# Performance work log

Measured on AMD Instinct MI355X. Metric: run time of the kernel, lower is better.

Reference implementation:

```python
import jax, jax.numpy as jnp
import numpy as np

B, TQ, TKV, D_MODEL, H, DQ, DV = 4, 2048, 2048, 1024, 16, 64, 64
DK = DQ

def setup_inputs() -> dict:
    key = jax.random.key(0)
    ks = jax.random.split(key, 8)
    s = 0.02
    return {
        "query_sequence": jax.random.normal(ks[0], (B, TQ, D_MODEL), jnp.float32),
        "key_value_sequence": jax.random.normal(ks[1], (B, TKV, D_MODEL), jnp.float32),
        "key_value_padding_mask": jnp.zeros((B, TKV), dtype=bool),
        "Wq": jax.random.normal(ks[2], (D_MODEL, H * DQ), jnp.float32) * s,
        "bq": jnp.zeros((H * DQ,), jnp.float32),
        "Wkv": jax.random.normal(ks[3], (D_MODEL, H * (DK + DV)), jnp.float32) * s,
        "bkv": jnp.zeros((H * (DK + DV),), jnp.float32),
        "Wo": jax.random.normal(ks[4], (H * DV, D_MODEL), jnp.float32) * s,
        "bo": jnp.zeros((D_MODEL,), jnp.float32),
        "apply_causal_mask": 1,
    }

def reference(query_sequence, key_value_sequence, key_value_padding_mask,
              Wq, bq, Wkv, bkv, Wo, bo, apply_causal_mask):
    b, tq, _ = query_sequence.shape
    tkv = key_value_sequence.shape[1]
    q = (query_sequence @ Wq + bq).reshape(b, tq, H, DQ)          # (B,Tq,H,Dq)
    kv = key_value_sequence @ Wkv + bkv
    k = kv[..., : H * DK].reshape(b, tkv, H, DK)                   # (B,Tkv,H,Dk)
    v = kv[..., H * DK :].reshape(b, tkv, H, DV)                   # (B,Tkv,H,Dv)
    scores = jnp.einsum("bqhd,bkhd->bhqk", q, k) / jnp.sqrt(jnp.float32(DK))
    neg_inf = jnp.float32(-jnp.inf)
    scores = jnp.where(key_value_padding_mask[:, None, None, :], neg_inf, scores)
    if apply_causal_mask:
        causal = jnp.tril(jnp.ones((tq, tkv), dtype=bool))
        scores = jnp.where(causal[None, None, :, :], scores, neg_inf)
    attn = jax.nn.softmax(scores, axis=-1)
    out = jnp.einsum("bhqk,bkhd->bqhd", attn, v).reshape(b, tq, H * DV)
    return out @ Wo + bo
```

## Files before the change

kernel.cpp:

```cpp
#include <hip/hip_runtime.h>
#include <hip/hip_bf16.h>

#define B_   4
#define TQ_  2048
#define TKV_ 2048
#define DM_  1024
#define H_   16
#define DH_  64

#define SC_FOLD 0.18033688011112042f

using f32x4  = __attribute__((ext_vector_type(4))) float;
using f32x16 = __attribute__((ext_vector_type(16))) float;
using s16x8  = __attribute__((ext_vector_type(8))) short;

static __device__ __forceinline__ unsigned short f2bf(float f) {
  union { float f; unsigned int u; } v; v.f = f;
  unsigned int r = v.u + 0x7FFFu + ((v.u >> 16) & 1u);
  return (unsigned short)(r >> 16);
}
static __device__ __forceinline__ unsigned int pk2(float a, float b) {
  unsigned int r;
  asm("v_cvt_pk_bf16_f32 %0, %1, %2" : "=v"(r) : "v"(a), "v"(b));
  return r;
}
static __device__ __forceinline__ float max3f(float a, float b, float c) {
  float r;
  asm("v_max3_f32 %0, %1, %2, %3" : "=v"(r) : "v"(a), "v"(b), "v"(c));
  return r;
}

#define GL16(g, l)                                                          \
  __builtin_amdgcn_global_load_lds(                                         \
      (const __attribute__((address_space(1))) unsigned int*)(g),           \
      (__attribute__((address_space(3))) unsigned int*)(l), 16, 0, 0)

static __device__ __forceinline__ void transpose_tile(
    const float* W, unsigned short* WT, int K, int N, int n0, int k0, float scale,
    float (*t)[65]) {
  int tx = threadIdx.x & 63, ty = threadIdx.x >> 6;
#pragma unroll
  for (int i = 0; i < 64; i += 4)
    t[ty + i][tx] = W[(size_t)(k0 + ty + i) * N + n0 + tx];
  __syncthreads();
#pragma unroll
  for (int i = 0; i < 64; i += 4)
    WT[(size_t)(n0 + ty + i) * K + k0 + tx] = f2bf(t[tx][ty + i] * scale);
}
static __device__ __forceinline__ void cast_gs(
    const float* in, unsigned short* out, int n4, int cb, int ncb) {
  for (int i = cb * 256 + threadIdx.x; i < n4; i += ncb * 256) {
    f32x4 v = *(const f32x4*)(in + (size_t)i * 4);
    unsigned long long u = (unsigned long long)pk2(v[0], v[1]) |
                           ((unsigned long long)pk2(v[2], v[3]) << 32);
    *(unsigned long long*)(out + (size_t)i * 4) = u;
  }
}

__global__ __launch_bounds__(256) void k_prep(
    const float* __restrict__ Wq, unsigned short* __restrict__ WqT,
    const float* __restrict__ Wkv, unsigned short* __restrict__ WkvT,
    const float* __restrict__ Wo, unsigned short* __restrict__ WoT,
    const float* __restrict__ xq, unsigned short* __restrict__ Aq,
    const float* __restrict__ xkv, unsigned short* __restrict__ Akv, int n4) {
  int bid = blockIdx.x;
  if (bid >= 3072) { cast_gs(xkv, Akv, n4, bid - 3072, 2048); return; }
  if (bid >= 1024) { cast_gs(xq, Aq, n4, bid - 1024, 2048); return; }
  __shared__ float t[64][65];
  if (bid < 256) {
    transpose_tile(Wq, WqT, 1024, 1024, (bid & 15) * 64, (bid >> 4) * 64, SC_FOLD, t);
  } else if (bid < 768) {
    int b2 = bid - 256;
    transpose_tile(Wkv, WkvT, 1024, 2048, (b2 & 31) * 64, (b2 >> 5) * 64, 1.0f, t);
  } else {
    int b2 = bid - 768;
    transpose_tile(Wo, WoT, 1024, 1024, (b2 & 15) * 64, (b2 >> 4) * 64, 1.0f, t);
  }
}

__global__ __launch_bounds__(256) void k_cast_bf16(
    const float* __restrict__ in, unsigned short* __restrict__ out, int n4) {
  cast_gs(in, out, n4, blockIdx.x, gridDim.x);
}

template <int MODE, int BN>
static __device__ __forceinline__ void gemm_body(
    const unsigned short* __restrict__ A, const unsigned short* __restrict__ BT,
    const float* __restrict__ bias, float bscale, unsigned short* __restrict__ out_a,
    unsigned short* __restrict__ out_b, float* __restrict__ out_f, int Kd,
    int bx, int by, unsigned short* As, unsigned short* Bs) {
  constexpr int NI = BN / 64;
  constexpr int NH = NI / 2;
  const int tid = threadIdx.x, lane = tid & 63, w = tid >> 6;
  const int wm = w >> 2, wn = w & 3;
  int m0 = by * 256, n0 = bx * BN;

  const int strow = tid >> 3;
  const int sx = ((tid & 7) << 4) ^ ((strow & 7) << 4);
  const char* gA = (const char*)(A + (size_t)(m0 + strow) * Kd) + sx;
  const char* gB = (const char*)(BT + (size_t)(n0 + strow) * Kd) + sx;
  char* lA = (char*)As;
  char* lB = (char*)Bs;

#define ST_A(bf, c, k0) \
  GL16(gA + ((size_t)(c) * 64 * Kd + (size_t)(k0)) * 2, lA + (bf) * 32768 + (c) * 8192 + tid * 16)
#define ST_B(bf, c, k0) \
  GL16(gB + ((size_t)(c) * 64 * Kd + (size_t)(k0)) * 2, lB + (bf) * (BN * 128) + (c) * 8192 + tid * 16)

  f32x4 acc[8][NI];
#pragma unroll
  for (int i = 0; i < 8; ++i)
#pragma unroll
    for (int j = 0; j < NI; ++j) acc[i][j] = (f32x4){0.f, 0.f, 0.f, 0.f};

  s16x8 afr[4][2], bfr[NI][2];
  const int arow = wm * 128 + (lane & 15);
  const int brow = wn * (NI * 16) + (lane & 15);
  const int fcol = (lane >> 4) * 16;

#define RD_A(bf, r) (*(const s16x8*)(lA + (bf) * 32768 + (r) * 128 + ((fcol + _kk * 64) ^ (((r) & 7) << 4))))
#define RD_B(bf, r) (*(const s16x8*)(lB + (bf) * (BN * 128) + (r) * 128 + ((fcol + _kk * 64) ^ (((r) & 7) << 4))))

  const int nT = Kd >> 6;

  ST_B(0, 0, 0); ST_B(0, 1, 0);
  if (BN == 256) { ST_B(0, 2, 0); ST_B(0, 3, 0); }
  ST_A(0, 0, 0); ST_A(0, 2, 0);
  ST_A(0, 1, 0); ST_A(0, 3, 0);
  asm volatile("s_waitcnt vmcnt(2)" ::: "memory");
  __builtin_amdgcn_s_barrier();

#pragma unroll 1
  for (int t = 0; t < nT; ++t) {
    const int cur = t & 1, nxt = cur ^ 1;
    const int k1 = (t + 1) << 6;
    const bool st = (t + 1 < nT);

#pragma unroll
    for (int mi = 0; mi < 4; ++mi)
#pragma unroll
      for (int _kk = 0; _kk < 2; ++_kk) afr[mi][_kk] = RD_A(cur, arow + mi * 16);
#pragma unroll
    for (int ni = 0; ni < NH; ++ni)
#pragma unroll
      for (int _kk = 0; _kk < 2; ++_kk) bfr[ni][_kk] = RD_B(cur, brow + ni * 16);
    if (st) { ST_B(nxt, 0, k1); ST_B(nxt, 1, k1); }
    __builtin_amdgcn_s_barrier();
    __builtin_amdgcn_s_setprio(1);
#pragma unroll
    for (int mi = 0; mi < 4; ++mi)
#pragma unroll
      for (int ni = 0; ni < NH; ++ni)
#pragma unroll
        for (int kk = 0; kk < 2; ++kk)
          acc[mi][ni] = __builtin_amdgcn_mfma_f32_16x16x32_bf16(afr[mi][kk], bfr[ni][kk], acc[mi][ni], 0, 0, 0);
    __builtin_amdgcn_s_setprio(0);
    __builtin_amdgcn_s_barrier();

#pragma unroll
    for (int ni = NH; ni < NI; ++ni)
#pragma unroll
      for (int _kk = 0; _kk < 2; ++_kk) bfr[ni][_kk] = RD_B(cur, brow + ni * 16);
    if (st) {
      if (BN == 256) { ST_B(nxt, 2, k1); ST_B(nxt, 3, k1); }
      else           { ST_A(nxt, 0, k1); ST_A(nxt, 2, k1); }
    }
    if (st) asm volatile("s_waitcnt vmcnt(4)" ::: "memory");
    else    asm volatile("s_waitcnt vmcnt(0)" ::: "memory");
    __builtin_amdgcn_s_barrier();
    __builtin_amdgcn_s_setprio(1);
#pragma unroll
    for (int mi = 0; mi < 4; ++mi)
#pragma unroll
      for (int ni = NH; ni < NI; ++ni)
#pragma unroll
        for (int kk = 0; kk < 2; ++kk)
          acc[mi][ni] = __builtin_amdgcn_mfma_f32_16x16x32_bf16(afr[mi][kk], bfr[ni][kk], acc[mi][ni], 0, 0, 0);
    __builtin_amdgcn_s_setprio(0);
    __builtin_amdgcn_s_barrier();

#pragma unroll
    for (int mi = 0; mi < 4; ++mi)
#pragma unroll
      for (int _kk = 0; _kk < 2; ++_kk) afr[mi][_kk] = RD_A(cur, arow + (mi + 4) * 16);
    if (st) {
      if (BN == 256) { ST_A(nxt, 0, k1); ST_A(nxt, 2, k1); }
      else           { ST_A(nxt, 1, k1); ST_A(nxt, 3, k1); }
    }
    __builtin_amdgcn_s_barrier();
    __builtin_amdgcn_s_setprio(1);
#pragma unroll
    for (int mi = 0; mi < 4; ++mi)
#pragma unroll
      for (int ni = 0; ni < NH; ++ni)
#pragma unroll
        for (int kk = 0; kk < 2; ++kk)
          acc[mi + 4][ni] = __builtin_amdgcn_mfma_f32_16x16x32_bf16(afr[mi][kk], bfr[ni][kk], acc[mi + 4][ni], 0, 0, 0);
    __builtin_amdgcn_s_setprio(0);
    __builtin_amdgcn_s_barrier();

    if (st && BN == 256) { ST_A(nxt, 1, k1); ST_A(nxt, 3, k1); }
    asm volatile("s_waitcnt vmcnt(2)" ::: "memory");
    __builtin_amdgcn_s_barrier();
    __builtin_amdgcn_s_setprio(1);
#pragma unroll
    for (int mi = 0; mi < 4; ++mi)
#pragma unroll
      for (int ni = NH; ni < NI; ++ni)
#pragma unroll
        for (int kk = 0; kk < 2; ++kk)
          acc[mi + 4][ni] = __builtin_amdgcn_mfma_f32_16x16x32_bf16(afr[mi][kk], bfr[ni][kk], acc[mi + 4][ni], 0, 0, 0);
    __builtin_amdgcn_s_setprio(0);
    __builtin_amdgcn_s_barrier();
  }

#pragma unroll
  for (int mi = 0; mi < 8; ++mi) {
#pragma unroll
    for (int ni = 0; ni < NI; ++ni) {
      int col = n0 + wn * (NI * 16) + ni * 16 + (lane & 15);
      int rbase = m0 + wm * 128 + mi * 16 + (lane >> 4) * 4;
      float bv = bias[col] * bscale;
      if (MODE == 1 && col >= H_ * DH_) {
        int c2 = col - H_ * DH_;
        int h = c2 >> 6, d = c2 & 63;
        int b = rbase >> 11, tt = rbase & 2047;
        union { unsigned short h4[4]; unsigned long long u; } p;
#pragma unroll
        for (int r = 0; r < 4; ++r) p.h4[r] = f2bf(acc[mi][ni][r] + bv);
        *(unsigned long long*)(out_b + ((((size_t)b * H_ + h) * DH_ + d) * TKV_ + tt)) = p.u;
      } else {
#pragma unroll
        for (int r = 0; r < 4; ++r) {
          float v = acc[mi][ni][r] + bv;
          int m = rbase + r;
          if (MODE == 0) {
            int b = m >> 11, tt = m & 2047;
            int h = col >> 6, d = col & 63;
            out_a[(((size_t)b * H_ + h) * TQ_ + tt) * DH_ + d] = f2bf(v);
          } else if (MODE == 1) {
            int b = m >> 11, tt = m & 2047;
            int h = col >> 6, d = col & 63;
            out_a[(((size_t)b * H_ + h) * TKV_ + tt) * DH_ + d] = f2bf(v);
          } else {
            out_f[(size_t)m * DM_ + col] = v;
          }
        }
      }
    }
  }
#undef ST_A
#undef ST_B
#undef RD_A
#undef RD_B
}

template <int MODE, int BN>
__global__ __launch_bounds__(512, 2) void k_gemm8(
    const unsigned short* __restrict__ A, const unsigned short* __restrict__ BT,
    const float* __restrict__ bias, float bscale, unsigned short* __restrict__ out_a,
    unsigned short* __restrict__ out_b, float* __restrict__ out_f, int Kd) {
  __shared__ __align__(16) unsigned short As[2 * 256 * 64];
  __shared__ __align__(16) unsigned short Bs[2 * BN * 64];
  int nwg = gridDim.x * gridDim.y;
  int bid = blockIdx.y * gridDim.x + blockIdx.x;
  int cpx = nwg >> 3;
  int sw = (bid & 7) * cpx + (bid >> 3);
  int bx = sw % gridDim.x, by = sw / gridDim.x;
  gemm_body<MODE, BN>(A, BT, bias, bscale, out_a, out_b, out_f, Kd, bx, by, As, Bs);
}

__global__ __launch_bounds__(512, 2) void k_gemm_qkv(
    const unsigned short* __restrict__ Aq, const unsigned short* __restrict__ WqT,
    const float* __restrict__ bq,
    const unsigned short* __restrict__ Akv, const unsigned short* __restrict__ WkvT,
    const float* __restrict__ bkv,
    unsigned short* __restrict__ Qb, unsigned short* __restrict__ Kb,
    unsigned short* __restrict__ Vb) {
  __shared__ __align__(16) unsigned short As[2 * 256 * 64];
  __shared__ __align__(16) unsigned short Bs[2 * 256 * 64];
  bool isQ = blockIdx.y < 32;
  int lby = isQ ? blockIdx.y : (blockIdx.y - 32);
  int bid = lby * 8 + blockIdx.x;
  int sw = (bid & 7) * 32 + (bid >> 3);
  int bx = sw & 7, by = sw >> 3;
  if (isQ)
    gemm_body<0, 128>(Aq, WqT, bq, SC_FOLD, Qb, nullptr, nullptr, 1024, bx, by, As, Bs);
  else
    gemm_body<1, 256>(Akv, WkvT, bkv, 1.0f, Kb, Vb, nullptr, 1024, bx, by, As, Bs);
}

__global__ __launch_bounds__(256, 2) void k_attn(
    const unsigned short* __restrict__ Qb, const unsigned short* __restrict__ Kb,
    const unsigned short* __restrict__ Vtb, const unsigned char* __restrict__ mask,
    const int* __restrict__ cflag, unsigned short* __restrict__ Ob) {
  __shared__ __align__(16) unsigned short Kt[2][128 * 64];
  __shared__ __align__(16) unsigned short Vt[2][64 * 128];
  __shared__ float bias_lds[2][128];
  __shared__ float red[4][32];
  __shared__ int s_any;

  int bid = blockIdx.y * gridDim.x + blockIdx.x;
  int r8 = bid & 7, q8 = bid >> 3;
  int bh = r8 * 8 + (q8 >> 3);
  int bx = q8 & 7;

  int b = bh >> 4, h = bh & 15;
  int tid = threadIdx.x, lane = tid & 63, w = tid >> 6;
  int hi = lane >> 5, l31 = lane & 31, l7 = lane & 7;
  const unsigned short* Qp = Qb + (size_t)bh * TQ_ * DH_;
  const char* Kp = (const char*)(Kb + (size_t)bh * TKV_ * DH_);
  const char* Vp = (const char*)(Vtb + (size_t)bh * DH_ * TKV_);
  const unsigned char* mp = mask + (size_t)b * TKV_;
  int causal = cflag[0];

  int st_r4 = tid >> 2;
  int st_c4 = (tid & 3) * 16;
  s16x8 pKr[4], pVr[4];

#define LOAD_KV(kv0)                                                          \
  {                                                                           \
    _Pragma("unroll")                                                         \
    for (int p = 0; p < 4; ++p) {                                             \
      int krow = (p >> 1) * 64 + st_r4;                                       \
      int kx = st_c4 + (p & 1) * 64;                                          \
      pKr[p] = *(const s16x8*)(Kp + ((size_t)((kv0) + krow) * 128 + kx));     \
      int vx = st_c4 + p * 64;                                                \
      pVr[p] = *(const s16x8*)(Vp + (((size_t)st_r4 * TKV_ + (kv0)) * 2 + vx)); \
    }                                                                         \
  }
#define WRITE_KV(bufi)                                                        \
  {                                                                           \
    char* kb_ = (char*)&Kt[bufi][0];                                          \
    char* vb_ = (char*)&Vt[bufi][0];                                          \
    _Pragma("unroll")                                                         \
    for (int p = 0; p < 4; ++p) {                                             \
      int krow = (p >> 1) * 64 + st_r4;                                       \
      int kx = st_c4 + (p & 1) * 64;                                          \
      *(s16x8*)(kb_ + krow * 128 + (kx ^ ((st_r4 & 7) << 4))) = pKr[p];       \
      int vx = st_c4 + p * 64;                                                \
      *(s16x8*)(vb_ + st_r4 * 256 + (vx ^ ((st_r4 & 7) << 4))) = pVr[p];      \
    }                                                                         \
  }

  if (tid == 0) s_any = 0;
  __syncthreads();
  {
    int any = 0;
    for (int i = tid; i < TKV_; i += 256) any |= mp[i];
    if (any) s_any = 1;
  }
  __syncthreads();
  const int has_mask = s_any;

#pragma unroll 1
  for (int pass = 0; pass < 2; ++pass) {
    int qb = (pass ? (15 - bx) : bx) * 128;
    int qw = qb + w * 32;
    int qrow = qw + l31;

    s16x8 bQ[4];
#pragma unroll
    for (int kk = 0; kk < 4; ++kk)
      bQ[kk] = *(const s16x8*)(Qp + (size_t)qrow * DH_ + kk * 16 + hi * 8);

    f32x16 accO[2];
#pragma unroll
    for (int i = 0; i < 16; ++i) { accO[0][i] = 0.f; accO[1][i] = 0.f; }
    float m_run = -INFINITY, l_run = 0.f;

    int nT = (causal ? (qb + 128) : TKV_) >> 7;

    LOAD_KV(0);
    WRITE_KV(0);
    if (has_mask && tid < 128) bias_lds[0][tid] = mp[tid] ? -1e30f : 0.0f;
    __syncthreads();

#pragma unroll 1
    for (int it = 0; it < nT; ++it) {
      int kv0 = it << 7;
      int cur = it & 1, nxt = cur ^ 1;
      if (it + 1 < nT) LOAD_KV(kv0 + 128);

      char* kbase = (char*)&Kt[cur][0];
      char* vbase = (char*)&Vt[cur][0];

      int nact = 4;
      if (causal) {
        int rem = qw + 31 - kv0;
        nact = rem < 0 ? 0 : ((rem >> 5) + 1);
        if (nact > 4) nact = 4;
      }

      if (nact > 0) {
        f32x16 sT[4];
        __builtin_amdgcn_s_setprio(1);
#pragma unroll
        for (int s = 0; s < 4; ++s) {
          if (s < nact) {
#pragma unroll
            for (int i = 0; i < 16; ++i) sT[s][i] = 0.f;
#pragma unroll
            for (int kk = 0; kk < 4; ++kk) {
              s16x8 aK = *(const s16x8*)(kbase + (s * 32 + l31) * 128 +
                                         ((kk * 32 + hi * 16) ^ (l7 << 4)));
              sT[s] = __builtin_amdgcn_mfma_f32_32x32x16_bf16(aK, bQ[kk], sT[s], 0, 0, 0);
            }
          }
        }
        __builtin_amdgcn_s_setprio(0);

        float a0 = -INFINITY, a1 = -INFINITY, a2 = -INFINITY, a3 = -INFINITY;
#pragma unroll
        for (int s = 0; s < 4; ++s) {
          if (s < nact) {
            int diag_s = causal && (kv0 + s * 32 + 31 > qw);
            if (diag_s || has_mask) {
#pragma unroll
              for (int r = 0; r < 16; ++r) {
                int kvloc = s * 32 + (r & 3) + 8 * (r >> 2) + 4 * hi;
                float sv = sT[s][r];
                if (has_mask) sv += bias_lds[cur][kvloc];
                if (diag_s && (kv0 + kvloc) > qrow) sv = -1e30f;
                sT[s][r] = sv;
              }
            }
#pragma unroll
            for (int r = 0; r < 16; r += 4) {
              a0 = fmaxf(a0, sT[s][r + 0]); a1 = fmaxf(a1, sT[s][r + 1]);
              a2 = fmaxf(a2, sT[s][r + 2]); a3 = fmaxf(a3, sT[s][r + 3]);
            }
          }
        }
        float mx = max3f(max3f(a0, a1, a2), a3, -3.0e30f);
        mx = fmaxf(mx, __shfl_xor(mx, 32));

        if (!__all(mx - m_run <= 8.0f)) {
          float mnew = fmaxf(m_run, mx);
          float sc_o = exp2f(m_run - mnew);
          m_run = mnew;
          l_run *= sc_o;
          red[w][l31] = sc_o;
#pragma unroll
          for (int r = 0; r < 16; ++r) {
            float f = red[w][(r & 3) + 8 * (r >> 2) + 4 * hi];
            accO[0][r] *= f;
            accO[1][r] *= f;
          }
        }

        float s0acc = 0.f, s1acc = 0.f, s2acc = 0.f, s3acc = 0.f;
#pragma unroll
        for (int s = 0; s < 4; ++s) {
          if (s < nact) {
#pragma unroll
            for (int r = 0; r < 16; r += 4) {
              float p0 = exp2f(sT[s][r + 0] - m_run);
              float p1 = exp2f(sT[s][r + 1] - m_run);
              float p2 = exp2f(sT[s][r + 2] - m_run);
              float p3 = exp2f(sT[s][r + 3] - m_run);
              sT[s][r + 0] = p0; sT[s][r + 1] = p1;
              sT[s][r + 2] = p2; sT[s][r + 3] = p3;
              s0acc += p0; s1acc += p1; s2acc += p2; s3acc += p3;
            }
          }
        }
        float ls = (s0acc + s1acc) + (s2acc + s3acc);
        ls += __shfl_xor(ls, 32);
        l_run += ls;

#pragma unroll
        for (int c = 0; c < 8; ++c) {
          if ((c >> 1) < nact) {
            int s = c >> 1, kk = c & 1;
            unsigned int x0 = pk2(sT[s][8 * kk + 0], sT[s][8 * kk + 1]);
            unsigned int y0 = pk2(sT[s][8 * kk + 2], sT[s][8 * kk + 3]);
            unsigned int x1 = pk2(sT[s][8 * kk + 4], sT[s][8 * kk + 5]);
            unsigned int y1 = pk2(sT[s][8 * kk + 6], sT[s][8 * kk + 7]);
            asm("v_permlane32_swap_b32 %0, %1" : "+v"(x0), "+v"(x1));
            asm("v_permlane32_swap_b32 %0, %1" : "+v"(y0), "+v"(y1));
            union { unsigned int u[4]; s16x8 v; } pf;
            pf.u[0] = x0;
            pf.u[1] = y0;
            pf.u[2] = x1;
            pf.u[3] = y1;
            __builtin_amdgcn_s_setprio(1);
#pragma unroll
            for (int dt = 0; dt < 2; ++dt) {
              s16x8 vf = *(const s16x8*)(vbase + (dt * 32 + l31) * 256 +
                                         ((c * 32 + hi * 16) ^ (l7 << 4)));
              accO[dt] = __builtin_amdgcn_mfma_f32_32x32x16_bf16(pf.v, vf, accO[dt], 0, 0, 0);
            }
            __builtin_amdgcn_s_setprio(0);
          }
        }
      }

      if (it + 1 < nT) {
        WRITE_KV(nxt);
        if (has_mask && tid < 128) bias_lds[nxt][tid] = mp[kv0 + 128 + tid] ? -1e30f : 0.0f;
      }
      __syncthreads();
    }

    red[w][l31] = 1.0f / l_run;
#pragma unroll
    for (int r = 0; r < 16; ++r) {
      int R = (r & 3) + 8 * (r >> 2) + 4 * hi;
      float f = red[w][R];
      int qg = qw + R;
      size_t base = ((size_t)b * TQ_ + qg) * DM_ + h * DH_ + l31;
      Ob[base] = f2bf(accO[0][r] * f);
      Ob[base + 32] = f2bf(accO[1][r] * f);
    }
  }
#undef LOAD_KV
#undef WRITE_KV
}

extern "C" void kernel_launch(void* const* d_in, const int* in_sizes, int n_in,
                              void* d_out, int out_size, void* d_ws, size_t ws_size,
                              hipStream_t stream) {
  const float* xq  = (const float*)d_in[0];
  const float* xkv = (const float*)d_in[1];
  const unsigned char* mask = (const unsigned char*)d_in[2];
  const float* Wq  = (const float*)d_in[3];
  const float* bq  = (const float*)d_in[4];
  const float* Wkv = (const float*)d_in[5];
  const float* bkv = (const float*)d_in[6];
  const float* Wo  = (const float*)d_in[7];
  const float* bo  = (const float*)d_in[8];
  const int* cflag = (const int*)d_in[9];
  float* out = (float*)d_out;

  char* ws = (char*)d_ws;
  unsigned short* WqT  = (unsigned short*)(ws);
  unsigned short* WkvT = (unsigned short*)(ws + ((size_t)2 << 20));
  unsigned short* WoT  = (unsigned short*)(ws + ((size_t)6 << 20));
  unsigned short* Qb   = (unsigned short*)(ws + ((size_t)8 << 20));
  unsigned short* Kb   = (unsigned short*)(ws + ((size_t)24 << 20));
  unsigned short* Vb   = (unsigned short*)(ws + ((size_t)40 << 20));
  unsigned short* Xr   = (unsigned short*)(ws + ((size_t)56 << 20));
  unsigned short* Ob   = Xr;
  const int n4 = B_ * TQ_ * DM_ / 4;

  if (ws_size >= ((size_t)88 << 20)) {
    unsigned short* Akv = (unsigned short*)(ws + ((size_t)72 << 20));
    k_prep<<<5120, 256, 0, stream>>>(Wq, WqT, Wkv, WkvT, Wo, WoT, xq, Xr, xkv, Akv, n4);
    k_gemm_qkv<<<dim3(8, 64), 512, 0, stream>>>(Xr, WqT, bq, Akv, WkvT, bkv, Qb, Kb, Vb);
    k_attn<<<dim3(8, B_ * H_), 256, 0, stream>>>(Qb, Kb, Vb, mask, cflag, Ob);
    k_gemm8<2, 128><<<dim3(8, 32), 512, 0, stream>>>(Ob, WoT, bo, 1.0f, nullptr, nullptr, out, 1024);
  } else {
    k_prep<<<3072, 256, 0, stream>>>(Wq, WqT, Wkv, WkvT, Wo, WoT, xq, Xr, xkv, nullptr, n4);
    k_gemm8<0, 128><<<dim3(8, 32), 512, 0, stream>>>(Xr, WqT, bq, SC_FOLD, Qb, nullptr, nullptr, 1024);
    k_cast_bf16<<<2048, 256, 0, stream>>>(xkv, Xr, n4);
    k_gemm8<1, 256><<<dim3(8, 32), 512, 0, stream>>>(Xr, WkvT, bkv, 1.0f, Kb, Vb, nullptr, 1024);
    k_attn<<<dim3(8, B_ * H_), 256, 0, stream>>>(Qb, Kb, Vb, mask, cflag, Ob);
    k_gemm8<2, 128><<<dim3(8, 32), 512, 0, stream>>>(Ob, WoT, bo, 1.0f, nullptr, nullptr, out, 1024);
  }
}
```

Before: 183.8 us.

## Split paired causal q-block passes into separate blocks and single-buffer K/V LDS

Each attention block used to process two mirrored q-blocks (bx and 15-bx) in sequence to balance causal work. Now each block handles one q-block, so the grid doubles to 16x64 blocks, and the K/V LDS tiles drop from double to single buffering with an extra barrier before each LDS write. Halving LDS use and doubling block count is meant to raise occupancy and parallelism. In exchange, blocks now carry uneven causal work and the extra barrier can expose global-load latency.

```diff
diff --git a/kernel.cpp b/kernel.cpp
--- a/kernel.cpp
+++ b/kernel.cpp
@@ -294,16 +294,16 @@
     const unsigned short* __restrict__ Qb, const unsigned short* __restrict__ Kb,
     const unsigned short* __restrict__ Vtb, const unsigned char* __restrict__ mask,
     const int* __restrict__ cflag, unsigned short* __restrict__ Ob) {
-  __shared__ __align__(16) unsigned short Kt[2][128 * 64];
-  __shared__ __align__(16) unsigned short Vt[2][64 * 128];
-  __shared__ float bias_lds[2][128];
+  __shared__ __align__(16) unsigned short Kt[128 * 64];
+  __shared__ __align__(16) unsigned short Vt[64 * 128];
+  __shared__ float bias_lds[128];
   __shared__ float red[4][32];
   __shared__ int s_any;
 
   int bid = blockIdx.y * gridDim.x + blockIdx.x;
   int r8 = bid & 7, q8 = bid >> 3;
-  int bh = r8 * 8 + (q8 >> 3);
-  int bx = q8 & 7;
+  int bh = r8 * 8 + (q8 >> 4);
+  int bx = q8 & 15;
 
   int b = bh >> 4, h = bh & 15;
   int tid = threadIdx.x, lane = tid & 63, w = tid >> 6;
@@ -313,6 +313,8 @@
   const char* Vp = (const char*)(Vtb + (size_t)bh * DH_ * TKV_);
   const unsigned char* mp = mask + (size_t)b * TKV_;
   int causal = cflag[0];
+  char* kbase = (char*)Kt;
+  char* vbase = (char*)Vt;
 
   int st_r4 = tid >> 2;
   int st_c4 = (tid & 3) * 16;
@@ -329,17 +331,15 @@
       pVr[p] = *(const s16x8*)(Vp + (((size_t)st_r4 * TKV_ + (kv0)) * 2 + vx)); \
     }                                                                         \
   }
-#define WRITE_KV(bufi)                                                        \
+#define WRITE_KV()                                                            \
   {                                                                           \
-    char* kb_ = (char*)&Kt[bufi][0];                                          \
-    char* vb_ = (char*)&Vt[bufi][0];                                          \
     _Pragma("unroll")                                                         \
     for (int p = 0; p < 4; ++p) {                                             \
       int krow = (p >> 1) * 64 + st_r4;                                       \
       int kx = st_c4 + (p & 1) * 64;                                          \
-      *(s16x8*)(kb_ + krow * 128 + (kx ^ ((st_r4 & 7) << 4))) = pKr[p];       \
+      *(s16x8*)(kbase + krow * 128 + (kx ^ ((st_r4 & 7) << 4))) = pKr[p];     \
       int vx = st_c4 + p * 64;                                                \
-      *(s16x8*)(vb_ + st_r4 * 256 + (vx ^ ((st_r4 & 7) << 4))) = pVr[p];      \
+      *(s16x8*)(vbase + st_r4 * 256 + (vx ^ ((st_r4 & 7) << 4))) = pVr[p];    \
     }                                                                         \
   }
 
@@ -353,166 +353,160 @@
   __syncthreads();
   const int has_mask = s_any;
 
+  int qb = bx * 128;
+  int qw = qb + w * 32;
+  int qrow = qw + l31;
+
+  s16x8 bQ[4];
+#pragma unroll
+  for (int kk = 0; kk < 4; ++kk)
+    bQ[kk] = *(const s16x8*)(Qp + (size_t)qrow * DH_ + kk * 16 + hi * 8);
+
+  f32x16 accO[2];
+#pragma unroll
+  for (int i = 0; i < 16; ++i) { accO[0][i] = 0.f; accO[1][i] = 0.f; }
+  float m_run = -INFINITY, l_run = 0.f;
+
+  int nT = (causal ? (qb + 128) : TKV_) >> 7;
+
+  LOAD_KV(0);
+  WRITE_KV();
+  if (has_mask && tid < 128) bias_lds[tid] = mp[tid] ? -1e30f : 0.0f;
+  __syncthreads();
+
 #pragma unroll 1
-  for (int pass = 0; pass < 2; ++pass) {
-    int qb = (pass ? (15 - bx) : bx) * 128;
-    int qw = qb + w * 32;
-    int qrow = qw + l31;
-
-    s16x8 bQ[4];
-#pragma unroll
-    for (int kk = 0; kk < 4; ++kk)
-      bQ[kk] = *(const s16x8*)(Qp + (size_t)qrow * DH_ + kk * 16 + hi * 8);
-
-    f32x16 accO[2];
-#pragma unroll
-    for (int i = 0; i < 16; ++i) { accO[0][i] = 0.f; accO[1][i] = 0.f; }
-    float m_run = -INFINITY, l_run = 0.f;
-
-    int nT = (causal ? (qb + 128) : TKV_) >> 7;
-
-    LOAD_KV(0);
-    WRITE_KV(0);
-    if (has_mask && tid < 128) bias_lds[0][tid] = mp[tid] ? -1e30f : 0.0f;
-    __syncthreads();
-
-#pragma unroll 1
-    for (int it = 0; it < nT; ++it) {
-      int kv0 = it << 7;
-      int cur = it & 1, nxt = cur ^ 1;
-      if (it + 1 < nT) LOAD_KV(kv0 + 128);
-
-      char* kbase = (char*)&Kt[cur][0];
-      char* vbase = (char*)&Vt[cur][0];
-
-      int nact = 4;
-      if (causal) {
-        int rem = qw + 31 - kv0;
-        nact = rem < 0 ? 0 : ((rem >> 5) + 1);
-        if (nact > 4) nact = 4;
-      }
-
-      if (nact > 0) {
-        f32x16 sT[4];
-        __builtin_amdgcn_s_setprio(1);
-#pragma unroll
-        for (int s = 0; s < 4; ++s) {
-          if (s < nact) {
-#pragma unroll
-            for (int i = 0; i < 16; ++i) sT[s][i] = 0.f;
-#pragma unroll
-            for (int kk = 0; kk < 4; ++kk) {
-              s16x8 aK = *(const s16x8*)(kbase + (s * 32 + l31) * 128 +
-                                         ((kk * 32 + hi * 16) ^ (l7 << 4)));
-              sT[s] = __builtin_amdgcn_mfma_f32_32x32x16_bf16(aK, bQ[kk], sT[s], 0, 0, 0);
-            }
-          }
-        }
-        __builtin_amdgcn_s_setprio(0);
-
-        float a0 = -INFINITY, a1 = -INFINITY, a2 = -INFINITY, a3 = -INFINITY;
-#pragma unroll
-        for (int s = 0; s < 4; ++s) {
-          if (s < nact) {
-            int diag_s = causal && (kv0 + s * 32 + 31 > qw);
-            if (diag_s || has_mask) {
-#pragma unroll
-              for (int r = 0; r < 16; ++r) {
-                int kvloc = s * 32 + (r & 3) + 8 * (r >> 2) + 4 * hi;
-                float sv = sT[s][r];
-                if (has_mask) sv += bias_lds[cur][kvloc];
-                if (diag_s && (kv0 + kvloc) > qrow) sv = -1e30f;
-                sT[s][r] = sv;
-              }
-            }
-#pragma unroll
-            for (int r = 0; r < 16; r += 4) {
-              a0 = fmaxf(a0, sT[s][r + 0]); a1 = fmaxf(a1, sT[s][r + 1]);
-              a2 = fmaxf(a2, sT[s][r + 2]); a3 = fmaxf(a3, sT[s][r + 3]);
-            }
-          }
-        }
-        float mx = max3f(max3f(a0, a1, a2), a3, -3.0e30f);
-        mx = fmaxf(mx, __shfl_xor(mx, 32));
-
-        if (!__all(mx - m_run <= 8.0f)) {
-          float mnew = fmaxf(m_run, mx);
-          float sc_o = exp2f(m_run - mnew);
-          m_run = mnew;
-          l_run *= sc_o;
-          red[w][l31] = sc_o;
-#pragma unroll
-          for (int r = 0; r < 16; ++r) {
-            float f = red[w][(r & 3) + 8 * (r >> 2) + 4 * hi];
-            accO[0][r] *= f;
-            accO[1][r] *= f;
-          }
-        }
-
-        float s0acc = 0.f, s1acc = 0.f, s2acc = 0.f, s3acc = 0.f;
-#pragma unroll
-        for (int s = 0; s < 4; ++s) {
-          if (s < nact) {
-#pragma unroll
-            for (int r = 0; r < 16; r += 4) {
-              float p0 = exp2f(sT[s][r + 0] - m_run);
-              float p1 = exp2f(sT[s][r + 1] - m_run);
-              float p2 = exp2f(sT[s][r + 2] - m_run);
-              float p3 = exp2f(sT[s][r + 3] - m_run);
-              sT[s][r + 0] = p0; sT[s][r + 1] = p1;
-              sT[s][r + 2] = p2; sT[s][r + 3] = p3;
-              s0acc += p0; s1acc += p1; s2acc += p2; s3acc += p3;
-            }
-          }
-        }
-        float ls = (s0acc + s1acc) + (s2acc + s3acc);
-        ls += __shfl_xor(ls, 32);
-        l_run += ls;
-
-#pragma unroll
-        for (int c = 0; c < 8; ++c) {
-          if ((c >> 1) < nact) {
-            int s = c >> 1, kk = c & 1;
-            unsigned int x0 = pk2(sT[s][8 * kk + 0], sT[s][8 * kk + 1]);
-            unsigned int y0 = pk2(sT[s][8 * kk + 2], sT[s][8 * kk + 3]);
-            unsigned int x1 = pk2(sT[s][8 * kk + 4], sT[s][8 * kk + 5]);
-            unsigned int y1 = pk2(sT[s][8 * kk + 6], sT[s][8 * kk + 7]);
-            asm("v_permlane32_swap_b32 %0, %1" : "+v"(x0), "+v"(x1));
-            asm("v_permlane32_swap_b32 %0, %1" : "+v"(y0), "+v"(y1));
-            union { unsigned int u[4]; s16x8 v; } pf;
-            pf.u[0] = x0;
-            pf.u[1] = y0;
-            pf.u[2] = x1;
-            pf.u[3] = y1;
-            __builtin_amdgcn_s_setprio(1);
-#pragma unroll
-            for (int dt = 0; dt < 2; ++dt) {
-              s16x8 vf = *(const s16x8*)(vbase + (dt * 32 + l31) * 256 +
-                                         ((c * 32 + hi * 16) ^ (l7 << 4)));
-              accO[dt] = __builtin_amdgcn_mfma_f32_32x32x16_bf16(pf.v, vf, accO[dt], 0, 0, 0);
-            }
-            __builtin_amdgcn_s_setprio(0);
+  for (int it = 0; it < nT; ++it) {
+    int kv0 = it << 7;
+    if (it + 1 < nT) LOAD_KV(kv0 + 128);
+
+    int nact = 4;
+    if (causal) {
+      int rem = qw + 31 - kv0;
+      nact = rem < 0 ? 0 : ((rem >> 5) + 1);
+      if (nact > 4) nact = 4;
+    }
+
+    if (nact > 0) {
+      f32x16 sT[4];
+      __builtin_amdgcn_s_setprio(1);
+#pragma unroll
+      for (int s = 0; s < 4; ++s) {
+        if (s < nact) {
+#pragma unroll
+          for (int i = 0; i < 16; ++i) sT[s][i] = 0.f;
+#pragma unroll
+          for (int kk = 0; kk < 4; ++kk) {
+            s16x8 aK = *(const s16x8*)(kbase + (s * 32 + l31) * 128 +
+                                       ((kk * 32 + hi * 16) ^ (l7 << 4)));
+            sT[s] = __builtin_amdgcn_mfma_f32_32x32x16_bf16(aK, bQ[kk], sT[s], 0, 0, 0);
           }
         }
       }
-
-      if (it + 1 < nT) {
-        WRITE_KV(nxt);
-        if (has_mask && tid < 128) bias_lds[nxt][tid] = mp[kv0 + 128 + tid] ? -1e30f : 0.0f;
+      __builtin_amdgcn_s_setprio(0);
+
+      float a0 = -INFINITY, a1 = -INFINITY, a2 = -INFINITY, a3 = -INFINITY;
+#pragma unroll
+      for (int s = 0; s < 4; ++s) {
+        if (s < nact) {
+          int diag_s = causal && (kv0 + s * 32 + 31 > qw);
+          if (diag_s || has_mask) {
+#pragma unroll
+            for (int r = 0; r < 16; ++r) {
+              int kvloc = s * 32 + (r & 3) + 8 * (r >> 2) + 4 * hi;
+              float sv = sT[s][r];
+              if (has_mask) sv += bias_lds[kvloc];
+              if (diag_s && (kv0 + kvloc) > qrow) sv = -1e30f;
+              sT[s][r] = sv;
+            }
+          }
+#pragma unroll
+          for (int r = 0; r < 16; r += 4) {
+            a0 = fmaxf(a0, sT[s][r + 0]); a1 = fmaxf(a1, sT[s][r + 1]);
+            a2 = fmaxf(a2, sT[s][r + 2]); a3 = fmaxf(a3, sT[s][r + 3]);
+          }
+        }
       }
-      __syncthreads();
+      float mx = max3f(max3f(a0, a1, a2), a3, -3.0e30f);
+      mx = fmaxf(mx, __shfl_xor(mx, 32));
+
+      if (!__all(mx - m_run <= 8.0f)) {
+        float mnew = fmaxf(m_run, mx);
+        float sc_o = exp2f(m_run - mnew);
+        m_run = mnew;
+        l_run *= sc_o;
+        red[w][l31] = sc_o;
+#pragma unroll
+        for (int r = 0; r < 16; ++r) {
+          float f = red[w][(r & 3) + 8 * (r >> 2) + 4 * hi];
+          accO[0][r] *= f;
+          accO[1][r] *= f;
+        }
+      }
+
+      float s0acc = 0.f, s1acc = 0.f, s2acc = 0.f, s3acc = 0.f;
+#pragma unroll
+      for (int s = 0; s < 4; ++s) {
+        if (s < nact) {
+#pragma unroll
+          for (int r = 0; r < 16; r += 4) {
+            float p0 = exp2f(sT[s][r + 0] - m_run);
+            float p1 = exp2f(sT[s][r + 1] - m_run);
+            float p2 = exp2f(sT[s][r + 2] - m_run);
+            float p3 = exp2f(sT[s][r + 3] - m_run);
+            sT[s][r + 0] = p0; sT[s][r + 1] = p1;
+            sT[s][r + 2] = p2; sT[s][r + 3] = p3;
+            s0acc += p0; s1acc += p1; s2acc += p2; s3acc += p3;
+          }
+        }
+      }
+      float ls = (s0acc + s1acc) + (s2acc + s3acc);
+      ls += __shfl_xor(ls, 32);
+      l_run += ls;
+
+#pragma unroll
+      for (int c = 0; c < 8; ++c) {
+        if ((c >> 1) < nact) {
+          int s = c >> 1, kk = c & 1;
+          unsigned int x0 = pk2(sT[s][8 * kk + 0], sT[s][8 * kk + 1]);
+          unsigned int y0 = pk2(sT[s][8 * kk + 2], sT[s][8 * kk + 3]);
+          unsigned int x1 = pk2(sT[s][8 * kk + 4], sT[s][8 * kk + 5]);
+          unsigned int y1 = pk2(sT[s][8 * kk + 6], sT[s][8 * kk + 7]);
+          asm("v_permlane32_swap_b32 %0, %1" : "+v"(x0), "+v"(x1));
+          asm("v_permlane32_swap_b32 %0, %1" : "+v"(y0), "+v"(y1));
+          union { unsigned int u[4]; s16x8 v; } pf;
+          pf.u[0] = x0;
+          pf.u[1] = y0;
+          pf.u[2] = x1;
+          pf.u[3] = y1;
+          __builtin_amdgcn_s_setprio(1);
+#pragma unroll
+          for (int dt = 0; dt < 2; ++dt) {
+            s16x8 vf = *(const s16x8*)(vbase + (dt * 32 + l31) * 256 +
+                                       ((c * 32 + hi * 16) ^ (l7 << 4)));
+            accO[dt] = __builtin_amdgcn_mfma_f32_32x32x16_bf16(pf.v, vf, accO[dt], 0, 0, 0);
+          }
+          __builtin_amdgcn_s_setprio(0);
+        }
+      }
     }
 
-    red[w][l31] = 1.0f / l_run;
-#pragma unroll
-    for (int r = 0; r < 16; ++r) {
-      int R = (r & 3) + 8 * (r >> 2) + 4 * hi;
-      float f = red[w][R];
-      int qg = qw + R;
-      size_t base = ((size_t)b * TQ_ + qg) * DM_ + h * DH_ + l31;
-      Ob[base] = f2bf(accO[0][r] * f);
-      Ob[base + 32] = f2bf(accO[1][r] * f);
+    __syncthreads();
+    if (it + 1 < nT) {
+      WRITE_KV();
+      if (has_mask && tid < 128) bias_lds[tid] = mp[kv0 + 128 + tid] ? -1e30f : 0.0f;
     }
+    __syncthreads();
+  }
+
+  red[w][l31] = 1.0f / l_run;
+#pragma unroll
+  for (int r = 0; r < 16; ++r) {
+    int R = (r & 3) + 8 * (r >> 2) + 4 * hi;
+    float f = red[w][R];
+    int qg = qw + R;
+    size_t base = ((size_t)b * TQ_ + qg) * DM_ + h * DH_ + l31;
+    Ob[base] = f2bf(accO[0][r] * f);
+    Ob[base + 32] = f2bf(accO[1][r] * f);
   }
 #undef LOAD_KV
 #undef WRITE_KV
@@ -548,14 +542,14 @@
     unsigned short* Akv = (unsigned short*)(ws + ((size_t)72 << 20));
     k_prep<<<5120, 256, 0, stream>>>(Wq, WqT, Wkv, WkvT, Wo, WoT, xq, Xr, xkv, Akv, n4);
     k_gemm_qkv<<<dim3(8, 64), 512, 0, stream>>>(Xr, WqT, bq, Akv, WkvT, bkv, Qb, Kb, Vb);
-    k_attn<<<dim3(8, B_ * H_), 256, 0, stream>>>(Qb, Kb, Vb, mask, cflag, Ob);
+    k_attn<<<dim3(16, B_ * H_), 256, 0, stream>>>(Qb, Kb, Vb, mask, cflag, Ob);
     k_gemm8<2, 128><<<dim3(8, 32), 512, 0, stream>>>(Ob, WoT, bo, 1.0f, nullptr, nullptr, out, 1024);
   } else {
     k_prep<<<3072, 256, 0, stream>>>(Wq, WqT, Wkv, WkvT, Wo, WoT, xq, Xr, xkv, nullptr, n4);
     k_gemm8<0, 128><<<dim3(8, 32), 512, 0, stream>>>(Xr, WqT, bq, SC_FOLD, Qb, nullptr, nullptr, 1024);
     k_cast_bf16<<<2048, 256, 0, stream>>>(xkv, Xr, n4);
     k_gemm8<1, 256><<<dim3(8, 32), 512, 0, stream>>>(Xr, WkvT, bkv, 1.0f, Kb, Vb, nullptr, 1024);
-    k_attn<<<dim3(8, B_ * H_), 256, 0, stream>>>(Qb, Kb, Vb, mask, cflag, Ob);
+    k_attn<<<dim3(16, B_ * H_), 256, 0, stream>>>(Qb, Kb, Vb, mask, cflag, Ob);
     k_gemm8<2, 128><<<dim3(8, 32), 512, 0, stream>>>(Ob, WoT, bo, 1.0f, nullptr, nullptr, out, 1024);
   }
 }
```

After: 215.9 us. 17.4% more time.
